# Optimization experiments

Measured on AMD Instinct MI355X. Metric: run time of the kernel, lower is better.

Reference implementation:

```python
import jax, jax.numpy as jnp
import numpy as np

K = 121          # kernel_size
C = 3            # channels
PAD = (K - 1) // 2  # 60, replicate padding so output matches input spatial size


def setup_inputs() -> dict:
    key = jax.random.key(0)
    k1, k2 = jax.random.split(key)
    x = jax.random.normal(k1, (8, C, 512, 512), dtype=jnp.float32)
    sigma = jax.random.uniform(k2, (), dtype=jnp.float32)
    return {"x": x, "sigma": sigma}


def _gaussian_kernel(sigma):
    # sigma -> sigma*8 + 16, variance = sigma**2 (as in torch forward)
    s = sigma * 8.0 + 16.0
    variance = s * s
    coord = jnp.arange(K, dtype=jnp.float32) - (K - 1) / 2.0  # centered coords
    diff = -(coord[:, None] ** 2 + coord[None, :] ** 2)       # [K,K], -((x-m)^2+(y-m)^2)
    kern = jnp.exp(diff / (2.0 * variance))
    # the 1/(2*pi*variance) prefactor cancels under normalization
    kern = kern / jnp.sum(kern)
    return kern


def reference(x, sigma):
    kern = _gaussian_kernel(sigma)
    # depthwise weights: [out_ch=C, in_ch/groups=1, K, K]
    w = jnp.broadcast_to(kern[None, None, :, :], (C, 1, K, K))
    # replicate padding (torch 'replicate' == jnp 'edge')
    xp = jnp.pad(x, ((0, 0), (0, 0), (PAD, PAD), (PAD, PAD)), mode="edge")
    out = jax.lax.conv_general_dilated(
        xp, w,
        window_strides=(1, 1),
        padding="VALID",
        dimension_numbers=("NCHW", "OIHW", "NCHW"),
        feature_group_count=C,
    )
    return out
```

## Files before the change

kernel.cpp:

```cpp
#include <hip/hip_runtime.h>


#define HH      512
#define WW      512
#define PLANE   (512 * 512)
#define NIMG    24
#define HPG_ROW 984

__device__ __forceinline__ void make_weights(const float* __restrict__ sigma,
                                             float* __restrict__ wlds, int tid) {
    const float s = sigma[0] * 8.0f + 16.0f;
    const float inv2v = 1.0f / (2.0f * s * s);
    float sum = 0.0f;
    #pragma unroll
    for (int k = 0; k <= 120; ++k) {
        const float c = (float)k - 60.0f;
        sum += __expf(-c * c * inv2v);
    }
    if (tid < 128) {
        float g = 0.0f;
        if (tid < 121) {
            const float c = (float)tid - 60.0f;
            g = __expf(-c * c * inv2v);
        }
        wlds[tid] = g / sum;
    }
}

#define V_OCT(CUR, NXT, KO)                                               \
    { *(float4*)&wq[0] = *(const float4*)&wlds[(KO) * 8];                 \
      *(float4*)&wq[4] = *(const float4*)&wlds[(KO) * 8 + 4];             \
      _Pragma("unroll")                                                   \
      for (int ki = 0; ki < 8; ++ki) {                                    \
          int rr = r0 - 52 + (KO) * 8 + ki;                               \
          rr = rr < 0 ? 0 : (rr > HH - 1 ? HH - 1 : rr);                  \
          NXT[ki] = *(const float2*)&src[(size_t)rr * WW];                \
          const float wk = wq[ki];                                        \
          _Pragma("unroll")                                               \
          for (int j = 0; j < 8; ++j) {                                   \
              const int idx = ki + j;                                     \
              const float2 v = (idx < 8) ? CUR[idx] : NXT[idx - 8];       \
              vac[j].x += wk * v.x; vac[j].y += wk * v.y;                 \
          }                                                               \
      }                                                                   \
    }

#define LOADG(DST, G)                                                     \
    { *(float4*)&DST[0] = *(const float4*)&bs[(G) * 12];                  \
      *(float4*)&DST[4] = *(const float4*)&bs[(G) * 12 + 4]; }

#define H_OCT2(A0, A1, A2, A3, B0, B1, B2, B3, KO)                        \
    { LOADG(A3, L + (KO) + 3)                                             \
      LOADG(B3, L + 32 + (KO) + 3)                                        \
      *(float4*)&wq[0] = *(const float4*)&wlds[(KO) * 8];                 \
      *(float4*)&wq[4] = *(const float4*)&wlds[(KO) * 8 + 4];             \
      _Pragma("unroll")                                                   \
      for (int ki = 0; ki < 8; ++ki) {                                    \
          const float wk = wq[ki];                                        \
          _Pragma("unroll")                                               \
          for (int j = 0; j < 8; ++j) {                                   \
              const int idx = ki + j;                                     \
              const float vA = (idx < 8) ? A0[idx]                        \
                             : (idx < 16) ? A1[idx - 8] : A2[idx - 16];   \
              const float vB = (idx < 8) ? B0[idx]                        \
                             : (idx < 16) ? B1[idx - 8] : B2[idx - 16];   \
              accA[j] += wk * vA;                                         \
              accB[j] += wk * vB;                                         \
          }                                                               \
      }                                                                   \
    }

__global__ __launch_bounds__(256, 4) void blur_fused(
        const float* __restrict__ x, const float* __restrict__ sigma,
        float* __restrict__ out) {
    __shared__ float sm[8 * HPG_ROW];
    __shared__ float wlds[128];
    const int tid = threadIdx.x;

    const int lid   = blockIdx.x + gridDim.x * blockIdx.y;
    const int tile  = (lid & 7) * 192 + (lid >> 3);
    const int r0    = (tile & 63) * 8;
    const int plane = tile >> 6;

    const int c0 = tid * 2;
    const float* __restrict__ src = x + (size_t)plane * PLANE + c0;

    float2 wa[8], wb[8], vac[8];
    float  wq[8];
    #pragma unroll
    for (int m = 0; m < 8; ++m) {
        int rr = r0 - 60 + m;
        rr = rr < 0 ? 0 : rr;
        wa[m] = *(const float2*)&src[(size_t)rr * WW];
    }
    make_weights(sigma, wlds, tid);
    #pragma unroll
    for (int j = 0; j < 8; ++j) vac[j] = make_float2(0.f, 0.f);
    __syncthreads();

    #pragma unroll 1
    for (int ko = 0; ko < 16; ko += 2) {
        V_OCT(wa, wb, ko)
        V_OCT(wb, wa, ko + 1)
    }

    {
        const int p  = c0 + 60;
        const int la = (p >> 3) * 12 + (p & 7);
        #pragma unroll
        for (int j = 0; j < 8; ++j)
            *(float2*)&sm[j * HPG_ROW + la] = vac[j];
    }
    __syncthreads();

    if (tid < 144) {
        int p, srca;
        if (tid < 60)       { p = tid;       srca = 7 * 12 + 4;  }
        else if (tid < 136) { p = 512 + tid; srca = 71 * 12 + 3; }
        else                { p = 512 + tid; srca = -1;          }
        const int dsta = (p >> 3) * 12 + (p & 7);
        #pragma unroll
        for (int r = 0; r < 8; ++r)
            sm[r * HPG_ROW + dsta] = (srca < 0) ? 0.0f
                                                : sm[r * HPG_ROW + srca];
    }
    __syncthreads();

    const int r = tid >> 5;
    const int L = tid & 31;
    const float* __restrict__ bs = sm + r * HPG_ROW;

    float a0[8], a1[8], a2[8], a3[8];
    float b0[8], b1[8], b2[8], b3[8];
    float accA[8], accB[8];
    #pragma unroll
    for (int j = 0; j < 8; ++j) { accA[j] = 0.0f; accB[j] = 0.0f; }

    LOADG(a0, L)      LOADG(b0, L + 32)
    LOADG(a1, L + 1)  LOADG(b1, L + 33)
    LOADG(a2, L + 2)  LOADG(b2, L + 34)

    #pragma unroll 1
    for (int ko = 0; ko < 16; ko += 4) {
        H_OCT2(a0, a1, a2, a3, b0, b1, b2, b3, ko)
        H_OCT2(a1, a2, a3, a0, b1, b2, b3, b0, ko + 1)
        H_OCT2(a2, a3, a0, a1, b2, b3, b0, b1, ko + 2)
        H_OCT2(a3, a0, a1, a2, b3, b0, b1, b2, ko + 3)
    }

    float* __restrict__ dst = out + (size_t)plane * PLANE
                                  + (size_t)(r0 + r) * WW + L * 8;
    *(float4*)(dst)        = make_float4(accA[0], accA[1], accA[2], accA[3]);
    *(float4*)(dst + 4)    = make_float4(accA[4], accA[5], accA[6], accA[7]);
    *(float4*)(dst + 256)  = make_float4(accB[0], accB[1], accB[2], accB[3]);
    *(float4*)(dst + 260)  = make_float4(accB[4], accB[5], accB[6], accB[7]);
}

extern "C" void kernel_launch(void* const* d_in, const int* in_sizes, int n_in,
                              void* d_out, int out_size, void* d_ws, size_t ws_size,
                              hipStream_t stream) {
    const float* x     = (const float*)d_in[0];
    const float* sigma = (const float*)d_in[1];
    float* out = (float*)d_out;
    blur_fused<<<dim3(HH / 8, NIMG), dim3(256), 0, stream>>>(x, sigma, out);
}
```

Measured before the change: 117.9 us.

## Interleave row halves in LDS, fold edge padding into writes, wave-reduce weights

Reorganizes the shared-memory layout so each thread's horizontal pass handles two columns 256 apart as float2 pairs. The vertical results are scattered directly into that interleaved layout, with replicate-padding values broadcast via shuffles, which removes one __syncthreads and the separate halo-fill pass. The weight normalization sum now uses a wave shuffle reduction instead of a 121-term serial loop, and launch bounds move to 5 waves per SIMD with a smaller LDS footprint. The added indexing and scattered scalar LDS stores could cause bank conflicts and extra instructions, and the tighter register budget risks spills.

```diff
diff --git a/kernel.cpp b/kernel.cpp
--- a/kernel.cpp
+++ b/kernel.cpp
@@ -1,25 +1,32 @@
 #include <hip/hip_runtime.h>
 
 
-#define HH      512
-#define WW      512
-#define PLANE   (512 * 512)
-#define NIMG    24
-#define HPG_ROW 984
+#define HH    512
+#define WW    512
+#define PLANE (512 * 512)
+#define NIMG  24
+#define SROW  960
+
+__device__ __forceinline__ int qla(int s) {
+    return 10 * (s >> 2) + 2 * (s & 3);
+}
 
 __device__ __forceinline__ void make_weights(const float* __restrict__ sigma,
                                              float* __restrict__ wlds, int tid) {
     const float s = sigma[0] * 8.0f + 16.0f;
     const float inv2v = 1.0f / (2.0f * s * s);
-    float sum = 0.0f;
+    const int lane = tid & 63;
+    const float c1 = (float)lane - 60.0f;
+    float sum = __expf(-c1 * c1 * inv2v);
+    if (lane + 64 <= 120) {
+        const float c2 = (float)(lane + 64) - 60.0f;
+        sum += __expf(-c2 * c2 * inv2v);
+    }
     #pragma unroll
-    for (int k = 0; k <= 120; ++k) {
-        const float c = (float)k - 60.0f;
-        sum += __expf(-c * c * inv2v);
-    }
+    for (int off = 1; off < 64; off <<= 1) sum += __shfl_xor(sum, off);
     if (tid < 128) {
         float g = 0.0f;
-        if (tid < 121) {
+        if (tid <= 120) {
             const float c = (float)tid - 60.0f;
             g = __expf(-c * c * inv2v);
         }
@@ -45,13 +52,19 @@
       }                                                                   \
     }
 
-#define LOADG(DST, G)                                                     \
-    { *(float4*)&DST[0] = *(const float4*)&bs[(G) * 12];                  \
-      *(float4*)&DST[4] = *(const float4*)&bs[(G) * 12 + 4]; }
+#define LOADW(DST, MB)                                                    \
+    { const int F = 20 * (L + (MB));                                      \
+      const float4 A = *(const float4*)&bs[F];                            \
+      const float4 Bq = *(const float4*)&bs[F + 4];                       \
+      const float4 Cq = *(const float4*)&bs[F + 10];                      \
+      const float4 Dq = *(const float4*)&bs[F + 14];                      \
+      DST[0] = make_float2(A.x, A.y);   DST[1] = make_float2(A.z, A.w);   \
+      DST[2] = make_float2(Bq.x, Bq.y); DST[3] = make_float2(Bq.z, Bq.w); \
+      DST[4] = make_float2(Cq.x, Cq.y); DST[5] = make_float2(Cq.z, Cq.w); \
+      DST[6] = make_float2(Dq.x, Dq.y); DST[7] = make_float2(Dq.z, Dq.w); }
 
-#define H_OCT2(A0, A1, A2, A3, B0, B1, B2, B3, KO)                        \
-    { LOADG(A3, L + (KO) + 3)                                             \
-      LOADG(B3, L + 32 + (KO) + 3)                                        \
+#define H_OCT(CUR, NXT, KO)                                               \
+    { LOADW(NXT, (KO) + 1)                                                \
       *(float4*)&wq[0] = *(const float4*)&wlds[(KO) * 8];                 \
       *(float4*)&wq[4] = *(const float4*)&wlds[(KO) * 8 + 4];             \
       _Pragma("unroll")                                                   \
@@ -60,20 +73,16 @@
           _Pragma("unroll")                                               \
           for (int j = 0; j < 8; ++j) {                                   \
               const int idx = ki + j;                                     \
-              const float vA = (idx < 8) ? A0[idx]                        \
-                             : (idx < 16) ? A1[idx - 8] : A2[idx - 16];   \
-              const float vB = (idx < 8) ? B0[idx]                        \
-                             : (idx < 16) ? B1[idx - 8] : B2[idx - 16];   \
-              accA[j] += wk * vA;                                         \
-              accB[j] += wk * vB;                                         \
+              const float2 v = (idx < 8) ? CUR[idx] : NXT[idx - 8];       \
+              hac[j].x += wk * v.x; hac[j].y += wk * v.y;                 \
           }                                                               \
       }                                                                   \
     }
 
-__global__ __launch_bounds__(256, 4) void blur_fused(
+__global__ __launch_bounds__(256, 5) void blur_fused(
         const float* __restrict__ x, const float* __restrict__ sigma,
         float* __restrict__ out) {
-    __shared__ float sm[8 * HPG_ROW];
+    __shared__ float sm[8 * SROW];
     __shared__ float wlds[128];
     const int tid = threadIdx.x;
 
@@ -105,55 +114,54 @@
     }
 
     {
-        const int p  = c0 + 60;
-        const int la = (p >> 3) * 12 + (p & 7);
+        const int laX0 = qla(c0 + 60), laX1 = qla(c0 + 61);
+        const int laY0 = qla(c0 - 196) + 1, laY1 = qla(c0 - 195) + 1;
         #pragma unroll
-        for (int j = 0; j < 8; ++j)
-            *(float2*)&sm[j * HPG_ROW + la] = vac[j];
+        for (int j = 0; j < 8; ++j) {
+            float* rp = sm + j * SROW;
+            if (c0 < 324) { rp[laX0] = vac[j].x; rp[laX1] = vac[j].y; }
+            if (c0 >= 196) { rp[laY0] = vac[j].x; rp[laY1] = vac[j].y; }
+        }
     }
-    __syncthreads();
-
-    if (tid < 144) {
-        int p, srca;
-        if (tid < 60)       { p = tid;       srca = 7 * 12 + 4;  }
-        else if (tid < 136) { p = 512 + tid; srca = 71 * 12 + 3; }
-        else                { p = 512 + tid; srca = -1;          }
-        const int dsta = (p >> 3) * 12 + (p & 7);
+    if (tid < 64) {
         #pragma unroll
-        for (int r = 0; r < 8; ++r)
-            sm[r * HPG_ROW + dsta] = (srca < 0) ? 0.0f
-                                                : sm[r * HPG_ROW + srca];
+        for (int j = 0; j < 8; ++j) {
+            const float lv = __shfl(vac[j].x, 0);
+            if (tid < 60) sm[j * SROW + qla(tid)] = lv;
+        }
+    } else if (tid >= 192) {
+        const int l = tid & 63;
+        #pragma unroll
+        for (int j = 0; j < 8; ++j) {
+            const float rv = __shfl(vac[j].y, 63);
+            sm[j * SROW + qla(316 + l) + 1] = rv;
+            if (l < 4) sm[j * SROW + qla(380 + l) + 1] = rv;
+        }
     }
     __syncthreads();
 
     const int r = tid >> 5;
     const int L = tid & 31;
-    const float* __restrict__ bs = sm + r * HPG_ROW;
+    const float* __restrict__ bs = sm + r * SROW;
 
-    float a0[8], a1[8], a2[8], a3[8];
-    float b0[8], b1[8], b2[8], b3[8];
-    float accA[8], accB[8];
+    float2 ha[8], hb[8], hac[8];
     #pragma unroll
-    for (int j = 0; j < 8; ++j) { accA[j] = 0.0f; accB[j] = 0.0f; }
+    for (int j = 0; j < 8; ++j) hac[j] = make_float2(0.f, 0.f);
 
-    LOADG(a0, L)      LOADG(b0, L + 32)
-    LOADG(a1, L + 1)  LOADG(b1, L + 33)
-    LOADG(a2, L + 2)  LOADG(b2, L + 34)
+    LOADW(ha, 0)
 
     #pragma unroll 1
-    for (int ko = 0; ko < 16; ko += 4) {
-        H_OCT2(a0, a1, a2, a3, b0, b1, b2, b3, ko)
-        H_OCT2(a1, a2, a3, a0, b1, b2, b3, b0, ko + 1)
-        H_OCT2(a2, a3, a0, a1, b2, b3, b0, b1, ko + 2)
-        H_OCT2(a3, a0, a1, a2, b3, b0, b1, b2, ko + 3)
+    for (int ko = 0; ko < 16; ko += 2) {
+        H_OCT(ha, hb, ko)
+        H_OCT(hb, ha, ko + 1)
     }
 
     float* __restrict__ dst = out + (size_t)plane * PLANE
                                   + (size_t)(r0 + r) * WW + L * 8;
-    *(float4*)(dst)        = make_float4(accA[0], accA[1], accA[2], accA[3]);
-    *(float4*)(dst + 4)    = make_float4(accA[4], accA[5], accA[6], accA[7]);
-    *(float4*)(dst + 256)  = make_float4(accB[0], accB[1], accB[2], accB[3]);
-    *(float4*)(dst + 260)  = make_float4(accB[4], accB[5], accB[6], accB[7]);
+    *(float4*)(dst)       = make_float4(hac[0].x, hac[1].x, hac[2].x, hac[3].x);
+    *(float4*)(dst + 4)   = make_float4(hac[4].x, hac[5].x, hac[6].x, hac[7].x);
+    *(float4*)(dst + 256) = make_float4(hac[0].y, hac[1].y, hac[2].y, hac[3].y);
+    *(float4*)(dst + 260) = make_float4(hac[4].y, hac[5].y, hac[6].y, hac[7].y);
 }
 
 extern "C" void kernel_launch(void* const* d_in, const int* in_sizes, int n_in,
```

Result: no change. 119.6 us (+1.5%).
